# Kernel optimization log

Hardware: AMD Instinct MI355X
Metric: run time of the kernel (lower is better)

Reference implementation:

```python
import jax, jax.numpy as jnp
import numpy as np

N, E, H, EF, DIM = 50000, 800000, 128, 16, 3
MF = 2 * H + EF + 1 + DIM  # dist_l2 (1) + dist_abs (DIM) = 276


def setup_inputs() -> dict:
    key = jax.random.key(0)
    ks = jax.random.split(key, 16)
    w = lambda k, shape, s=0.05: (jax.random.normal(k, shape, jnp.float32) * s)
    return dict(
        h=jax.random.normal(ks[0], (N, H), jnp.float32),
        coords=jax.random.normal(ks[1], (N, DIM), jnp.float32),
        a=jax.random.normal(ks[2], (E, EF), jnp.float32),
        src=jax.random.randint(ks[3], (E,), 0, N),
        dst=jax.random.randint(ks[4], (E,), 0, N),
        We1=w(ks[5], (MF, H)), be1=jnp.zeros((H,), jnp.float32),
        We2=w(ks[6], (H, H)), be2=jnp.zeros((H,), jnp.float32),
        Wa=w(ks[7], (H, 1)), ba=jnp.zeros((1,), jnp.float32),
        Wn1=w(ks[8], (2 * H, H)), bn1=jnp.zeros((H,), jnp.float32),
        Wn2=w(ks[9], (H, H)), bn2=jnp.zeros((H,), jnp.float32),
        Wc1=w(ks[10], (MF, H)), bc1=jnp.zeros((H,), jnp.float32),
        Wc2=w(ks[11], (H, H)), bc2=jnp.zeros((H,), jnp.float32),
        Wc3=w(ks[12], (H, 1), 0.001),  # xavier gain=0.001, no bias
    )


def reference(h, coords, a, src, dst,
              We1, be1, We2, be2, Wa, ba,
              Wn1, bn1, Wn2, bn2,
              Wc1, bc1, Wc2, bc2, Wc3):
    act = jax.nn.silu
    # gather node data onto edges
    xs, xd = coords[src], coords[dst]          # [E, DIM]
    diffs = xs - xd                            # [E, DIM]
    radials = jnp.linalg.norm(diffs, axis=-1, keepdims=True)  # dist_l2
    D = jnp.concatenate([radials, jnp.abs(diffs)], axis=-1)   # dist_l2, dist_abs
    f = jnp.concatenate([h[src], h[dst], D, a], axis=-1)      # [E, MF]
    # coord_mlp: Lin-act-Lin-act-Lin(no bias)
    cm = act(f @ Wc1 + bc1)
    cm = act(cm @ Wc2 + bc2)
    cm = cm @ Wc3                              # [E, 1]
    msg_x = cm * diffs / (radials + 1.0)       # [E, DIM]
    # edge_mlp + attention gate
    mh = act(f @ We1 + be1)
    mh = act(mh @ We2 + be2)                   # [E, H]
    att = jax.nn.sigmoid(mh @ Wa + ba)         # [E, 1]
    msg_h = att * mh
    # scatter-sum to destination nodes
    x_agg = jax.ops.segment_sum(msg_x, dst, num_segments=N)
    h_agg = jax.ops.segment_sum(msg_h, dst, num_segments=N)
    coords_out = coords + x_agg
    nh = act(jnp.concatenate([h, h_agg], axis=-1) @ Wn1 + bn1) @ Wn2 + bn2
    h_out = h + nh
    return h_out, coords_out
```

## Files before the change

kernel.cpp:

```cpp
#include <hip/hip_runtime.h>
#include <math.h>

#define HH 128
#define HP 64

typedef __attribute__((ext_vector_type(8))) short short8;
typedef __attribute__((ext_vector_type(4))) float float4v;
typedef __attribute__((ext_vector_type(4))) unsigned uint4v;

__device__ __forceinline__ float blo(unsigned w){ return __uint_as_float(w << 16); }
__device__ __forceinline__ float bhi(unsigned w){ return __uint_as_float(w & 0xffff0000u); }
__device__ __forceinline__ unsigned short f2b(float x){
  unsigned u = __float_as_uint(x);
  u += 0x7fffu + ((u >> 16) & 1u);
  return (unsigned short)(u >> 16);
}
__device__ __forceinline__ unsigned pack2(float a, float b){
  return (unsigned)f2b(a) | ((unsigned)f2b(b) << 16);
}
__device__ __forceinline__ float silu_f(float x){ return x / (1.f + __expf(-x)); }

__global__ __launch_bounds__(256, 2) void precompute_mfma_kernel(
    const float* __restrict__ h,
    const float* __restrict__ We1, const float* __restrict__ be1,
    const float* __restrict__ Wc1, const float* __restrict__ bc1,
    unsigned* __restrict__ A1, unsigned* __restrict__ B1,
    unsigned* __restrict__ Ac, unsigned* __restrict__ Bc, int N)
{
  __shared__ unsigned short hs[2][16 * 136];

  const int t = threadIdx.x;
  const int lane = t & 63;
  const int w = t >> 6;
  const int col = lane & 15;
  const int quad = lane >> 4;

  const float* Wsel = (w < 2) ? We1 : Wc1;
  const int kb = (w & 1) * 128;
  unsigned* outp = (w == 0) ? A1 : (w == 1) ? B1 : (w == 2) ? Ac : Bc;
  const float* biasp = (w == 0) ? be1 : (w == 2) ? bc1 : nullptr;

  uint4v wf[8][4];
  #pragma unroll
  for (int nt = 0; nt < 8; ++nt) {
    const int cn = nt * 16 + col;
    #pragma unroll
    for (int ks = 0; ks < 4; ++ks) {
      unsigned u[4];
      #pragma unroll
      for (int i = 0; i < 4; ++i) {
        const int k0 = kb + ks * 32 + quad * 8 + 2 * i;
        u[i] = pack2(Wsel[(size_t)k0 * 128 + cn], Wsel[(size_t)(k0 + 1) * 128 + cn]);
      }
      wf[nt][ks] = (uint4v){u[0], u[1], u[2], u[3]};
    }
  }
  float bias[8];
  #pragma unroll
  for (int nt = 0; nt < 8; ++nt) bias[nt] = biasp ? biasp[nt * 16 + col] : 0.f;

  const int ntiles = (N + 15) >> 4;
  auto stage = [&](int tl, int b) {
    const int n0s = tl * 16;
    for (int idx = t; idx < 16 * 64; idx += 256) {
      const int row = idx >> 6, jp = idx & 63;
      const int n = min(n0s + row, N - 1);
      float2 hv = ((const float2*)h)[(size_t)n * 64 + jp];
      ((unsigned*)&hs[b][row * 136])[jp] = pack2(hv.x, hv.y);
    }
  };

  int tile = blockIdx.x;
  if (tile < ntiles) stage(tile, 0);
  int buf = 0;
  for (; tile < ntiles; tile += gridDim.x, buf ^= 1) {
    __syncthreads();
    if (tile + (int)gridDim.x < ntiles) stage(tile + gridDim.x, buf ^ 1);

    float4v acc[8] = {{0,0,0,0},{0,0,0,0},{0,0,0,0},{0,0,0,0},
                      {0,0,0,0},{0,0,0,0},{0,0,0,0},{0,0,0,0}};
    #pragma unroll
    for (int ks = 0; ks < 4; ++ks) {
      short8 af = __builtin_bit_cast(short8,
          *(const uint4v*)&hs[buf][col * 136 + ks * 32 + quad * 8]);
      #pragma unroll
      for (int nt = 0; nt < 8; ++nt)
        acc[nt] = __builtin_amdgcn_mfma_f32_16x16x32_bf16(
            af, __builtin_bit_cast(short8, wf[nt][ks]), acc[nt], 0, 0, 0);
    }
    const int n0 = tile * 16;
    #pragma unroll
    for (int nt = 0; nt < 8; ++nt) {
      #pragma unroll
      for (int r = 0; r < 4; ++r) {
        float v = acc[nt][r] + bias[nt];
        float o = __shfl_xor(v, 1, 64);
        const int node = n0 + quad * 4 + r;
        if (!(lane & 1) && node < N)
          outp[(size_t)node * HP + (nt >> 2) * 32 + ((col >> 1) << 2) + (nt & 3)]
              = pack2(v, o);
      }
    }
  }
}

template<int MODE>
__global__ __launch_bounds__(256, 3) void edge_kernel(
    const unsigned* __restrict__ Apart, const unsigned* __restrict__ Bpart,
    const float* __restrict__ W1,
    const float* __restrict__ W2, const float* __restrict__ b2,
    const float* __restrict__ Wv,
    const float* __restrict__ ba_p,
    const int* __restrict__ src, const int* __restrict__ dst,
    const float* __restrict__ coords, const float* __restrict__ afeat,
    float* __restrict__ out_agg, int E)
{
  __shared__ unsigned short W2Ts[128 * 136];
  __shared__ unsigned short mhl16[32 * 136];
  __shared__ unsigned short tailsA[3][32 * 40];
  __shared__ float    dif[3][32 * 4];
  __shared__ int      sl[3][32], dl[3][32];
  __shared__ float    p_lds[4][16];

  const int t = threadIdx.x;
  const int lane = t & 63;
  const int w = t >> 6;
  const int mtile = w >> 1;
  const int nhalf = w & 1;
  const int col = lane & 15;
  const int quad = lane >> 4;

  for (int i = t; i < 128 * 128; i += 256) {
    int k = i >> 7, n = i & 127;
    W2Ts[n * 136 + k] = f2b(W2[i]);
  }
  for (int i = t; i < 3 * 32 * 20; i += 256) ((unsigned*)tailsA)[i] = 0u;

  uint4v wtf[4];
  #pragma unroll
  for (int nt = 0; nt < 4; ++nt) {
    const int n = nhalf * 64 + nt * 16 + col;
    unsigned u[4];
    #pragma unroll
    for (int i = 0; i < 4; ++i) {
      const int k0 = quad * 8 + 2 * i;
      float a = (k0     < 20) ? W1[(size_t)(256 + k0    ) * 128 + n] : 0.f;
      float b = (k0 + 1 < 20) ? W1[(size_t)(256 + k0 + 1) * 128 + n] : 0.f;
      u[i] = pack2(a, b);
    }
    wtf[nt] = (uint4v){u[0], u[1], u[2], u[3]};
  }
  float b2reg[4], wvreg[4];
  #pragma unroll
  for (int nt = 0; nt < 4; ++nt) {
    const int n = (nhalf * 4 + nt) * 16 + col;
    b2reg[nt] = b2[n];
    wvreg[nt] = Wv[n];
  }
  const float bav = (MODE == 0) ? ba_p[0] : 0.f;

  auto stage = [&](int tl, int b) {
    const int e0s = tl * 32;
    if (t < 32) {
      int eg = e0s + t;
      int s = 0, d = 0;
      if (eg < E) { s = src[eg]; d = dst[eg]; }
      sl[b][t] = s; dl[b][t] = d;
      float dx = coords[s*3+0] - coords[d*3+0];
      float dy = coords[s*3+1] - coords[d*3+1];
      float dz = coords[s*3+2] - coords[d*3+2];
      float rad = sqrtf(dx*dx + dy*dy + dz*dz);
      dif[b][t*4+0] = dx; dif[b][t*4+1] = dy;
      dif[b][t*4+2] = dz; dif[b][t*4+3] = rad;
      unsigned* ta = (unsigned*)&tailsA[b][t * 40];
      ta[0] = pack2(rad, fabsf(dx));
      ta[1] = pack2(fabsf(dy), fabsf(dz));
    }
    if (t < 128) {
      int e = t >> 2, q4 = t & 3;
      int eg = e0s + e;
      float4 v = make_float4(0.f, 0.f, 0.f, 0.f);
      if (eg < E) v = ((const float4*)afeat)[(size_t)eg * 4 + q4];
      unsigned* d4 = (unsigned*)&tailsA[b][e * 40 + 4 + q4 * 4];
      d4[0] = pack2(v.x, v.y);
      d4[1] = pack2(v.z, v.w);
    }
  };

  const int gs = gridDim.x;
  const int ntiles = (E + 31) >> 5;
  const int T0 = blockIdx.x;
  if (T0 < ntiles)      stage(T0, 0);
  if (T0 + gs < ntiles) stage(T0 + gs, 1);
  __syncthreads();

  uint4v wa4[4], wb4[4];
  const int jb4 = nhalf * 32 + ((col >> 1) << 2);
  auto issueG = [&](int b) {
    #pragma unroll
    for (int r = 0; r < 4; ++r) {
      const int e = mtile * 16 + quad * 4 + r;
      wa4[r] = *(const uint4v*)(Apart + (size_t)sl[b][e] * HP + jb4);
      wb4[r] = *(const uint4v*)(Bpart + (size_t)dl[b][e] * HP + jb4);
    }
  };
  if (T0 < ntiles) issueG(0);

  int buf = 0;
  for (int tile = T0; tile < ntiles; tile += gs, buf = (buf == 2) ? 0 : buf + 1) {
    const int e0 = tile * 32;

    float4v acct[4] = {{0,0,0,0},{0,0,0,0},{0,0,0,0},{0,0,0,0}};
    {
      const unsigned short* ap = &tailsA[buf][(mtile * 16 + col) * 40 + quad * 8];
      short8 af = __builtin_bit_cast(short8, *(const uint4v*)ap);
      #pragma unroll
      for (int nt = 0; nt < 4; ++nt)
        acct[nt] = __builtin_amdgcn_mfma_f32_16x16x32_bf16(
            af, __builtin_bit_cast(short8, wtf[nt]), acct[nt], 0, 0, 0);
    }

    const bool hiSel = (col & 1);
    #pragma unroll
    for (int r = 0; r < 4; ++r) {
      const int er_ = mtile * 16 + quad * 4 + r;
      #pragma unroll
      for (int nt = 0; nt < 4; ++nt) {
        unsigned ua = wa4[r][nt], ub = wb4[r][nt];
        float va = hiSel ? bhi(ua) : blo(ua);
        float vb = hiSel ? bhi(ub) : blo(ub);
        float v = va + vb + acct[nt][r];
        mhl16[er_ * 136 + nhalf * 64 + nt * 16 + col] = f2b(silu_f(v));
      }
    }
    __syncthreads();

    if (tile + 2 * gs < ntiles) stage(tile + 2 * gs, (buf == 0) ? 2 : buf - 1);

    float4v acc[4] = {{0,0,0,0},{0,0,0,0},{0,0,0,0},{0,0,0,0}};
    {
      const unsigned short* abase = &mhl16[(mtile * 16 + col) * 136 + quad * 8];
      #pragma unroll
      for (int ks = 0; ks < 4; ++ks) {
        short8 af = __builtin_bit_cast(short8, *(const uint4v*)(abase + ks * 32));
        #pragma unroll
        for (int nt = 0; nt < 4; ++nt) {
          const unsigned short* bp =
              &W2Ts[((nhalf * 4 + nt) * 16 + col) * 136 + ks * 32 + quad * 8];
          short8 bf = __builtin_bit_cast(short8, *(const uint4v*)bp);
          acc[nt] = __builtin_amdgcn_mfma_f32_16x16x32_bf16(af, bf, acc[nt], 0, 0, 0);
        }
      }
    }

    float p[4] = {0.f, 0.f, 0.f, 0.f};
    #pragma unroll
    for (int nt = 0; nt < 4; ++nt)
      #pragma unroll
      for (int r = 0; r < 4; ++r) {
        float v = silu_f(acc[nt][r] + b2reg[nt]);
        acc[nt][r] = v;
        p[r] += v * wvreg[nt];
      }
    #pragma unroll
    for (int r = 0; r < 4; ++r) {
      #pragma unroll
      for (int off = 1; off < 16; off <<= 1) p[r] += __shfl_xor(p[r], off, 64);
    }
    if (col == 0) {
      #pragma unroll
      for (int r = 0; r < 4; ++r) p_lds[w][quad * 4 + r] = p[r];
    }
    __syncthreads();

    if (tile + gs < ntiles) issueG((buf == 2) ? 0 : buf + 1);

    #pragma unroll
    for (int r = 0; r < 4; ++r) {
      const int le = quad * 4 + r;
      const int ei = mtile * 16 + le;
      const int eg = e0 + ei;
      const float pfull = p_lds[w][le] + p_lds[w ^ 1][le];
      if (MODE == 0) {
        if (eg < E) {
          float att = 1.f / (1.f + __expf(-(pfull + bav)));
          int d = dl[buf][ei];
          #pragma unroll
          for (int nt = 0; nt < 4; ++nt) {
            int n = (nhalf * 4 + nt) * 16 + col;
            unsafeAtomicAdd(&out_agg[(size_t)d * HH + n], att * acc[nt][r]);
          }
        }
      } else {
        if (nhalf == 0 && eg < E && col < 3) {
          float rad = dif[buf][ei * 4 + 3];
          float fac = pfull / (rad + 1.f);
          unsafeAtomicAdd(&out_agg[(size_t)dl[buf][ei] * 3 + col],
                          fac * dif[buf][ei * 4 + col]);
        }
      }
    }
  }
}

__global__ __launch_bounds__(256, 4) void node_l1_mfma(
    const float* __restrict__ h, const float* __restrict__ h_agg,
    const float* __restrict__ Wn1, const float* __restrict__ bn1,
    unsigned* __restrict__ g, int N)
{
  __shared__ unsigned short xs[2][16 * 264];

  const int t = threadIdx.x;
  const int lane = t & 63;
  const int w = t >> 6;
  const int col = lane & 15;
  const int quad = lane >> 4;
  const int wbase = w * 32;

  uint4v wf[2][8];
  #pragma unroll
  for (int nt = 0; nt < 2; ++nt) {
    const int cn = wbase + nt * 16 + col;
    #pragma unroll
    for (int ks = 0; ks < 8; ++ks) {
      unsigned u[4];
      #pragma unroll
      for (int i = 0; i < 4; ++i) {
        const int k0 = ks * 32 + quad * 8 + 2 * i;
        u[i] = pack2(Wn1[(size_t)k0 * 128 + cn], Wn1[(size_t)(k0 + 1) * 128 + cn]);
      }
      wf[nt][ks] = (uint4v){u[0], u[1], u[2], u[3]};
    }
  }
  float bias[2] = { bn1[wbase + col], bn1[wbase + 16 + col] };

  const int ntiles = (N + 15) >> 4;
  auto stage = [&](int tl, int b) {
    const int n0s = tl * 16;
    for (int idx = t; idx < 16 * 128; idx += 256) {
      const int row = idx >> 7, jp = idx & 127;
      const int n = min(n0s + row, N - 1);
      float2 v = (jp < 64) ? ((const float2*)h)[(size_t)n * 64 + jp]
                           : ((const float2*)h_agg)[(size_t)n * 64 + (jp - 64)];
      ((unsigned*)&xs[b][row * 264])[jp] = pack2(v.x, v.y);
    }
  };

  int tile = blockIdx.x;
  if (tile < ntiles) stage(tile, 0);
  int buf = 0;
  for (; tile < ntiles; tile += gridDim.x, buf ^= 1) {
    __syncthreads();
    if (tile + (int)gridDim.x < ntiles) stage(tile + gridDim.x, buf ^ 1);

    float4v acc[2] = {{0,0,0,0},{0,0,0,0}};
    #pragma unroll
    for (int ks = 0; ks < 8; ++ks) {
      short8 af = __builtin_bit_cast(short8,
          *(const uint4v*)&xs[buf][col * 264 + ks * 32 + quad * 8]);
      acc[0] = __builtin_amdgcn_mfma_f32_16x16x32_bf16(
          af, __builtin_bit_cast(short8, wf[0][ks]), acc[0], 0, 0, 0);
      acc[1] = __builtin_amdgcn_mfma_f32_16x16x32_bf16(
          af, __builtin_bit_cast(short8, wf[1][ks]), acc[1], 0, 0, 0);
    }
    const int n0 = tile * 16;
    #pragma unroll
    for (int nt = 0; nt < 2; ++nt) {
      #pragma unroll
      for (int r = 0; r < 4; ++r) {
        float v = silu_f(acc[nt][r] + bias[nt]);
        float o = __shfl_xor(v, 1, 64);
        const int node = n0 + quad * 4 + r;
        if (!(lane & 1) && node < N)
          g[(size_t)node * HP + ((wbase + nt * 16 + col) >> 1)] = pack2(v, o);
      }
    }
  }
}

__global__ __launch_bounds__(256, 4) void node_l2_mfma(
    const unsigned* __restrict__ g, const float* __restrict__ h,
    const float* __restrict__ Wn2, const float* __restrict__ bn2,
    float* __restrict__ hout, int N)
{
  const int t = threadIdx.x;
  const int lane = t & 63;
  const int w = t >> 6;
  const int col = lane & 15;
  const int quad = lane >> 4;
  const int wbase = w * 32;

  uint4v wf[2][4];
  #pragma unroll
  for (int nt = 0; nt < 2; ++nt) {
    const int cn = wbase + nt * 16 + col;
    #pragma unroll
    for (int ks = 0; ks < 4; ++ks) {
      unsigned u[4];
      #pragma unroll
      for (int i = 0; i < 4; ++i) {
        const int k0 = ks * 32 + quad * 8 + 2 * i;
        u[i] = pack2(Wn2[(size_t)k0 * 128 + cn], Wn2[(size_t)(k0 + 1) * 128 + cn]);
      }
      wf[nt][ks] = (uint4v){u[0], u[1], u[2], u[3]};
    }
  }
  float bias[2] = { bn2[wbase + col], bn2[wbase + 16 + col] };

  const int ntiles = (N + 15) >> 4;
  for (int tile = blockIdx.x; tile < ntiles; tile += gridDim.x) {
    const int n0 = tile * 16;
    const int na = min(n0 + col, N - 1);

    float4v acc[2] = {{0,0,0,0},{0,0,0,0}};
    #pragma unroll
    for (int ks = 0; ks < 4; ++ks) {
      short8 af = __builtin_bit_cast(short8,
          *(const uint4v*)(g + (size_t)na * HP + ks * 16 + quad * 4));
      acc[0] = __builtin_amdgcn_mfma_f32_16x16x32_bf16(
          af, __builtin_bit_cast(short8, wf[0][ks]), acc[0], 0, 0, 0);
      acc[1] = __builtin_amdgcn_mfma_f32_16x16x32_bf16(
          af, __builtin_bit_cast(short8, wf[1][ks]), acc[1], 0, 0, 0);
    }
    #pragma unroll
    for (int nt = 0; nt < 2; ++nt) {
      const int cn = wbase + nt * 16 + col;
      #pragma unroll
      for (int r = 0; r < 4; ++r) {
        const int node = n0 + quad * 4 + r;
        if (node < N) {
          float v = acc[nt][r] + bias[nt] + h[(size_t)node * HH + cn];
          hout[(size_t)node * HH + cn] = v;
        }
      }
    }
  }
}

__global__ void coords_out_kernel(const float* __restrict__ coords,
                                  const float* __restrict__ x_agg,
                                  float* __restrict__ out, int n3)
{
  int i = blockIdx.x * blockDim.x + threadIdx.x;
  if (i < n3) out[i] = coords[i] + x_agg[i];
}

extern "C" void kernel_launch(void* const* d_in, const int* in_sizes, int n_in,
                              void* d_out, int out_size, void* d_ws, size_t ws_size,
                              hipStream_t stream)
{
  const float* h      = (const float*)d_in[0];
  const float* coords = (const float*)d_in[1];
  const float* afeat  = (const float*)d_in[2];
  const int*   src    = (const int*)d_in[3];
  const int*   dst    = (const int*)d_in[4];
  const float* We1 = (const float*)d_in[5];
  const float* be1 = (const float*)d_in[6];
  const float* We2 = (const float*)d_in[7];
  const float* be2 = (const float*)d_in[8];
  const float* Wa  = (const float*)d_in[9];
  const float* ba  = (const float*)d_in[10];
  const float* Wn1 = (const float*)d_in[11];
  const float* bn1 = (const float*)d_in[12];
  const float* Wn2 = (const float*)d_in[13];
  const float* bn2 = (const float*)d_in[14];
  const float* Wc1 = (const float*)d_in[15];
  const float* bc1 = (const float*)d_in[16];
  const float* Wc2 = (const float*)d_in[17];
  const float* bc2 = (const float*)d_in[18];
  const float* Wc3 = (const float*)d_in[19];

  const int E = in_sizes[3];
  const int N = in_sizes[0] / HH;

  unsigned* A1 = (unsigned*)d_ws;
  unsigned* B1 = A1 + (size_t)N * HP;
  unsigned* Ac = B1 + (size_t)N * HP;
  unsigned* Bc = Ac + (size_t)N * HP;
  float* h_agg = (float*)(Bc + (size_t)N * HP);
  float* x_agg = h_agg + (size_t)N * HH;
  unsigned* gbuf = A1;

  hipMemsetAsync(h_agg, 0, ((size_t)N * HH + (size_t)N * 3) * sizeof(float), stream);

  precompute_mfma_kernel<<<512, 256, 0, stream>>>(h, We1, be1, Wc1, bc1,
                                                  A1, B1, Ac, Bc, N);

  edge_kernel<0><<<768, 256, 0, stream>>>(A1, B1, We1, We2, be2, Wa, ba,
                                          src, dst, coords, afeat, h_agg, E);
  edge_kernel<1><<<768, 256, 0, stream>>>(Ac, Bc, Wc1, Wc2, bc2, Wc3, nullptr,
                                          src, dst, coords, afeat, x_agg, E);

  node_l1_mfma<<<512, 256, 0, stream>>>(h, h_agg, Wn1, bn1, gbuf, N);
  node_l2_mfma<<<1024, 256, 0, stream>>>(gbuf, h, Wn2, bn2, (float*)d_out, N);
  coords_out_kernel<<<(N * 3 + 255) / 256, 256, 0, stream>>>(
      coords, x_agg, (float*)d_out + (size_t)N * HH, N * 3);
}
```

Before: 785.8 us.

## Double edge tile size and prefetch node gathers two tiles ahead

The edge kernel now runs 512-thread blocks on 64-edge tiles, so each block's one-off W2 transpose into LDS is spread over more edges. The main loop is unrolled by two with two register sets for the A/B node-row gathers. Gathers are issued two tiles ahead to hide the latency of the random global loads. The cost is more registers, and the tighter launch bound (512, 4) could force spills. Larger LDS buffers may also limit how many blocks fit per CU.

Measured after the change: 927.8 us. 1.18x slower.

```diff
diff --git a/kernel.cpp b/kernel.cpp
--- a/kernel.cpp
+++ b/kernel.cpp
@@ -104,8 +104,104 @@
   }
 }
 
+
+#define EDGE_ITER(TILE, BUF, WA, WB)                                            \
+  {                                                                             \
+    const int e0 = (TILE) * 64;                                                 \
+                        \
+    float4v acct[4] = {{0,0,0,0},{0,0,0,0},{0,0,0,0},{0,0,0,0}};                \
+    {                                                                           \
+      const unsigned short* ap =                                                \
+          &tailsA[(BUF)][(mtile * 16 + col) * 40 + quad * 8];                   \
+      short8 af = __builtin_bit_cast(short8, *(const uint4v*)ap);               \
+      _Pragma("unroll")                                                         \
+      for (int nt = 0; nt < 4; ++nt)                                            \
+        acct[nt] = __builtin_amdgcn_mfma_f32_16x16x32_bf16(                     \
+            af, __builtin_bit_cast(short8, wtf[nt]), acct[nt], 0, 0, 0);        \
+    }                                                                           \
+                       \
+    _Pragma("unroll")                                                           \
+    for (int r = 0; r < 4; ++r) {                                               \
+      const int er_ = mtile * 16 + quad * 4 + r;                                \
+      _Pragma("unroll")                                                         \
+      for (int nt = 0; nt < 4; ++nt) {                                          \
+        unsigned ua = WA[r][nt], ub = WB[r][nt];                                \
+        float va = hiSel ? bhi(ua) : blo(ua);                                   \
+        float vb = hiSel ? bhi(ub) : blo(ub);                                   \
+        float v = va + vb + acct[nt][r];                                        \
+        mhl16[er_ * 136 + nhalf * 64 + nt * 16 + col] = f2b(silu_f(v));         \
+      }                                                                         \
+    }                                                                           \
+    __syncthreads(); \
+    if ((TILE) + 2 * gs < ntiles) stage((TILE) + 2 * gs, ((BUF) + 2) % 3);      \
+                                                 \
+    float4v acc[4] = {{0,0,0,0},{0,0,0,0},{0,0,0,0},{0,0,0,0}};                 \
+    {                                                                           \
+      const unsigned short* abase = &mhl16[(mtile * 16 + col) * 136 + quad * 8];\
+      _Pragma("unroll")                                                         \
+      for (int ks = 0; ks < 4; ++ks) {                                          \
+        short8 af = __builtin_bit_cast(short8, *(const uint4v*)(abase + ks*32));\
+        _Pragma("unroll")                                                       \
+        for (int nt = 0; nt < 4; ++nt) {                                        \
+          const unsigned short* bp =                                            \
+              &W2Ts[((nhalf * 4 + nt) * 16 + col) * 136 + ks * 32 + quad * 8];  \
+          short8 bf = __builtin_bit_cast(short8, *(const uint4v*)bp);           \
+          acc[nt] = __builtin_amdgcn_mfma_f32_16x16x32_bf16(af, bf, acc[nt],    \
+                                                            0, 0, 0);           \
+        }                                                                       \
+      }                                                                         \
+    }                                                                           \
+                        \
+    float p[4] = {0.f, 0.f, 0.f, 0.f};                                          \
+    _Pragma("unroll")                                                           \
+    for (int nt = 0; nt < 4; ++nt)                                              \
+      _Pragma("unroll")                                                         \
+      for (int r = 0; r < 4; ++r) {                                             \
+        float v = silu_f(acc[nt][r] + b2reg[nt]);                               \
+        acc[nt][r] = v;                                                         \
+        p[r] += v * wvreg[nt];                                                  \
+      }                                                                         \
+    _Pragma("unroll")                                                           \
+    for (int r = 0; r < 4; ++r) {                                               \
+      _Pragma("unroll")                                                         \
+      for (int off = 1; off < 16; off <<= 1) p[r] += __shfl_xor(p[r], off, 64); \
+    }                                                                           \
+    if (col == 0) {                                                             \
+      _Pragma("unroll")                                                         \
+      for (int r = 0; r < 4; ++r) p_lds[w][quad * 4 + r] = p[r];                \
+    }                                                                           \
+    __syncthreads();                        \
+    if ((TILE) + 2 * gs < ntiles) issueG(((BUF) + 2) % 3, WA, WB);              \
+                                                                   \
+    _Pragma("unroll")                                                           \
+    for (int r = 0; r < 4; ++r) {                                               \
+      const int le = quad * 4 + r;                                              \
+      const int ei = mtile * 16 + le;                                           \
+      const int eg = e0 + ei;                                                   \
+      const float pfull = p_lds[w][le] + p_lds[w ^ 1][le];                      \
+      if (MODE == 0) {                                                          \
+        if (eg < E) {                                                           \
+          float att = 1.f / (1.f + __expf(-(pfull + bav)));                     \
+          int d = dl[(BUF)][ei];                                                \
+          _Pragma("unroll")                                                     \
+          for (int nt = 0; nt < 4; ++nt) {                                      \
+            int n = (nhalf * 4 + nt) * 16 + col;                                \
+            unsafeAtomicAdd(&out_agg[(size_t)d * HH + n], att * acc[nt][r]);    \
+          }                                                                     \
+        }                                                                       \
+      } else {                                                                  \
+        if (nhalf == 0 && eg < E && col < 3) {                                  \
+          float rad = dif[(BUF)][ei * 4 + 3];                                   \
+          float fac = pfull / (rad + 1.f);                                      \
+          unsafeAtomicAdd(&out_agg[(size_t)dl[(BUF)][ei] * 3 + col],            \
+                          fac * dif[(BUF)][ei * 4 + col]);                      \
+        }                                                                       \
+      }                                                                         \
+    }                                                                           \
+  }
+
 template<int MODE>
-__global__ __launch_bounds__(256, 3) void edge_kernel(
+__global__ __launch_bounds__(512, 4) void edge_kernel(
     const unsigned* __restrict__ Apart, const unsigned* __restrict__ Bpart,
     const float* __restrict__ W1,
     const float* __restrict__ W2, const float* __restrict__ b2,
@@ -116,11 +212,11 @@
     float* __restrict__ out_agg, int E)
 {
   __shared__ unsigned short W2Ts[128 * 136];
-  __shared__ unsigned short mhl16[32 * 136];
-  __shared__ unsigned short tailsA[3][32 * 40];
-  __shared__ float    dif[3][32 * 4];
-  __shared__ int      sl[3][32], dl[3][32];
-  __shared__ float    p_lds[4][16];
+  __shared__ unsigned short mhl16[64 * 136];
+  __shared__ unsigned short tailsA[3][64 * 40];
+  __shared__ float    dif[3][64 * 4];
+  __shared__ int      sl[3][64], dl[3][64];
+  __shared__ float    p_lds[8][16];
 
   const int t = threadIdx.x;
   const int lane = t & 63;
@@ -130,11 +226,11 @@
   const int col = lane & 15;
   const int quad = lane >> 4;
 
-  for (int i = t; i < 128 * 128; i += 256) {
+  for (int i = t; i < 128 * 128; i += 512) {
     int k = i >> 7, n = i & 127;
     W2Ts[n * 136 + k] = f2b(W2[i]);
   }
-  for (int i = t; i < 3 * 32 * 20; i += 256) ((unsigned*)tailsA)[i] = 0u;
+  for (int i = t; i < 3 * 64 * 20; i += 512) ((unsigned*)tailsA)[i] = 0u;
 
   uint4v wtf[4];
   #pragma unroll
@@ -158,10 +254,12 @@
     wvreg[nt] = Wv[n];
   }
   const float bav = (MODE == 0) ? ba_p[0] : 0.f;
+  const bool hiSel = (col & 1);
+  const int jb4 = nhalf * 32 + ((col >> 1) << 2);
 
   auto stage = [&](int tl, int b) {
-    const int e0s = tl * 32;
-    if (t < 32) {
+    const int e0s = tl * 64;
+    if (t < 64) {
       int eg = e0s + t;
       int s = 0, d = 0;
       if (eg < E) { s = src[eg]; d = dst[eg]; }
@@ -176,7 +274,7 @@
       ta[0] = pack2(rad, fabsf(dx));
       ta[1] = pack2(fabsf(dy), fabsf(dz));
     }
-    if (t < 128) {
+    if (t < 256) {
       int e = t >> 2, q4 = t & 3;
       int eg = e0s + e;
       float4 v = make_float4(0.f, 0.f, 0.f, 0.f);
@@ -187,119 +285,35 @@
     }
   };
 
+  auto issueG = [&](int b, uint4v (&A)[4], uint4v (&B)[4]) {
+    #pragma unroll
+    for (int r = 0; r < 4; ++r) {
+      const int e = mtile * 16 + quad * 4 + r;
+      A[r] = *(const uint4v*)(Apart + (size_t)sl[b][e] * HP + jb4);
+      B[r] = *(const uint4v*)(Bpart + (size_t)dl[b][e] * HP + jb4);
+    }
+  };
+
   const int gs = gridDim.x;
-  const int ntiles = (E + 31) >> 5;
+  const int ntiles = (E + 63) >> 6;
   const int T0 = blockIdx.x;
   if (T0 < ntiles)      stage(T0, 0);
   if (T0 + gs < ntiles) stage(T0 + gs, 1);
   __syncthreads();
 
-  uint4v wa4[4], wb4[4];
-  const int jb4 = nhalf * 32 + ((col >> 1) << 2);
-  auto issueG = [&](int b) {
-    #pragma unroll
-    for (int r = 0; r < 4; ++r) {
-      const int e = mtile * 16 + quad * 4 + r;
-      wa4[r] = *(const uint4v*)(Apart + (size_t)sl[b][e] * HP + jb4);
-      wb4[r] = *(const uint4v*)(Bpart + (size_t)dl[b][e] * HP + jb4);
-    }
-  };
-  if (T0 < ntiles) issueG(0);
-
+  uint4v wa0[4], wb0[4], wa1[4], wb1[4];
+  if (T0 < ntiles)      issueG(0, wa0, wb0);
+  if (T0 + gs < ntiles) issueG(1, wa1, wb1);
+
+  int tile = T0;
   int buf = 0;
-  for (int tile = T0; tile < ntiles; tile += gs, buf = (buf == 2) ? 0 : buf + 1) {
-    const int e0 = tile * 32;
-
-    float4v acct[4] = {{0,0,0,0},{0,0,0,0},{0,0,0,0},{0,0,0,0}};
-    {
-      const unsigned short* ap = &tailsA[buf][(mtile * 16 + col) * 40 + quad * 8];
-      short8 af = __builtin_bit_cast(short8, *(const uint4v*)ap);
-      #pragma unroll
-      for (int nt = 0; nt < 4; ++nt)
-        acct[nt] = __builtin_amdgcn_mfma_f32_16x16x32_bf16(
-            af, __builtin_bit_cast(short8, wtf[nt]), acct[nt], 0, 0, 0);
-    }
-
-    const bool hiSel = (col & 1);
-    #pragma unroll
-    for (int r = 0; r < 4; ++r) {
-      const int er_ = mtile * 16 + quad * 4 + r;
-      #pragma unroll
-      for (int nt = 0; nt < 4; ++nt) {
-        unsigned ua = wa4[r][nt], ub = wb4[r][nt];
-        float va = hiSel ? bhi(ua) : blo(ua);
-        float vb = hiSel ? bhi(ub) : blo(ub);
-        float v = va + vb + acct[nt][r];
-        mhl16[er_ * 136 + nhalf * 64 + nt * 16 + col] = f2b(silu_f(v));
-      }
-    }
-    __syncthreads();
-
-    if (tile + 2 * gs < ntiles) stage(tile + 2 * gs, (buf == 0) ? 2 : buf - 1);
-
-    float4v acc[4] = {{0,0,0,0},{0,0,0,0},{0,0,0,0},{0,0,0,0}};
-    {
-      const unsigned short* abase = &mhl16[(mtile * 16 + col) * 136 + quad * 8];
-      #pragma unroll
-      for (int ks = 0; ks < 4; ++ks) {
-        short8 af = __builtin_bit_cast(short8, *(const uint4v*)(abase + ks * 32));
-        #pragma unroll
-        for (int nt = 0; nt < 4; ++nt) {
-          const unsigned short* bp =
-              &W2Ts[((nhalf * 4 + nt) * 16 + col) * 136 + ks * 32 + quad * 8];
-          short8 bf = __builtin_bit_cast(short8, *(const uint4v*)bp);
-          acc[nt] = __builtin_amdgcn_mfma_f32_16x16x32_bf16(af, bf, acc[nt], 0, 0, 0);
-        }
-      }
-    }
-
-    float p[4] = {0.f, 0.f, 0.f, 0.f};
-    #pragma unroll
-    for (int nt = 0; nt < 4; ++nt)
-      #pragma unroll
-      for (int r = 0; r < 4; ++r) {
-        float v = silu_f(acc[nt][r] + b2reg[nt]);
-        acc[nt][r] = v;
-        p[r] += v * wvreg[nt];
-      }
-    #pragma unroll
-    for (int r = 0; r < 4; ++r) {
-      #pragma unroll
-      for (int off = 1; off < 16; off <<= 1) p[r] += __shfl_xor(p[r], off, 64);
-    }
-    if (col == 0) {
-      #pragma unroll
-      for (int r = 0; r < 4; ++r) p_lds[w][quad * 4 + r] = p[r];
-    }
-    __syncthreads();
-
-    if (tile + gs < ntiles) issueG((buf == 2) ? 0 : buf + 1);
-
-    #pragma unroll
-    for (int r = 0; r < 4; ++r) {
-      const int le = quad * 4 + r;
-      const int ei = mtile * 16 + le;
-      const int eg = e0 + ei;
-      const float pfull = p_lds[w][le] + p_lds[w ^ 1][le];
-      if (MODE == 0) {
-        if (eg < E) {
-          float att = 1.f / (1.f + __expf(-(pfull + bav)));
-          int d = dl[buf][ei];
-          #pragma unroll
-          for (int nt = 0; nt < 4; ++nt) {
-            int n = (nhalf * 4 + nt) * 16 + col;
-            unsafeAtomicAdd(&out_agg[(size_t)d * HH + n], att * acc[nt][r]);
-          }
-        }
-      } else {
-        if (nhalf == 0 && eg < E && col < 3) {
-          float rad = dif[buf][ei * 4 + 3];
-          float fac = pfull / (rad + 1.f);
-          unsafeAtomicAdd(&out_agg[(size_t)dl[buf][ei] * 3 + col],
-                          fac * dif[buf][ei * 4 + col]);
-        }
-      }
-    }
+  for (; tile + gs < ntiles; tile += 2 * gs) {
+    EDGE_ITER(tile,      buf,           wa0, wb0);
+    EDGE_ITER(tile + gs, (buf + 1) % 3, wa1, wb1);
+    buf = (buf + 2) % 3;
+  }
+  if (tile < ntiles) {
+    EDGE_ITER(tile, buf, wa0, wb0);
   }
 }
 
@@ -486,9 +500,9 @@
   precompute_mfma_kernel<<<512, 256, 0, stream>>>(h, We1, be1, Wc1, bc1,
                                                   A1, B1, Ac, Bc, N);
 
-  edge_kernel<0><<<768, 256, 0, stream>>>(A1, B1, We1, We2, be2, Wa, ba,
+  edge_kernel<0><<<512, 512, 0, stream>>>(A1, B1, We1, We2, be2, Wa, ba,
                                           src, dst, coords, afeat, h_agg, E);
-  edge_kernel<1><<<768, 256, 0, stream>>>(Ac, Bc, Wc1, Wc2, bc2, Wc3, nullptr,
+  edge_kernel<1><<<512, 512, 0, stream>>>(Ac, Bc, Wc1, Wc2, bc2, Wc3, nullptr,
                                           src, dst, coords, afeat, x_agg, E);
 
   node_l1_mfma<<<512, 256, 0, stream>>>(h, h_agg, Wn1, bn1, gbuf, N);
```
